# Kernel optimization log

Hardware: AMD Instinct MI355X
Metric: run time of the kernel (lower is better)

The kernel has to match this reference:

```python
import jax, jax.numpy as jnp
import numpy as np

N, E, D, K = 32768, 16384, 4, 8          # nodes, hyperedges, edges/node, nodes/edge
IN_DIM, OUT_DIM, EDGE_DIM, NUM_HEADS = 128, 128, 64, 8


def setup_inputs() -> dict:
    key = jax.random.key(0)
    ks = jax.random.split(key, 16)
    s_in = 1.0 / np.sqrt(IN_DIM)
    s_out = 1.0 / np.sqrt(OUT_DIM)
    s_edge = 1.0 / np.sqrt(EDGE_DIM)
    return {
        "x": jax.random.normal(ks[0], (N, IN_DIM), jnp.float32),
        "edge_attr": jax.random.normal(ks[1], (E, EDGE_DIM), jnp.float32),
        "node_edges": jax.random.randint(ks[2], (N, D), 0, E),   # hyperedges containing each node
        "edge_nodes": jax.random.randint(ks[3], (E, K), 0, N),   # nodes inside each hyperedge
        "W_lin": jax.random.normal(ks[4], (OUT_DIM, IN_DIM), jnp.float32) * s_in,
        "W_edge": jax.random.normal(ks[5], (OUT_DIM, EDGE_DIM), jnp.float32) * s_edge,
        "Wq": jax.random.normal(ks[6], (OUT_DIM, OUT_DIM), jnp.float32) * s_out,
        "Wk": jax.random.normal(ks[7], (OUT_DIM, OUT_DIM), jnp.float32) * s_out,
        "Wv": jax.random.normal(ks[8], (OUT_DIM, OUT_DIM), jnp.float32) * s_out,
        "bq": jnp.zeros((OUT_DIM,), jnp.float32),
        "bk": jnp.zeros((OUT_DIM,), jnp.float32),
        "bv": jnp.zeros((OUT_DIM,), jnp.float32),
        "Wo": jax.random.normal(ks[9], (OUT_DIM, OUT_DIM), jnp.float32) * s_out,
        "bo": jnp.zeros((OUT_DIM,), jnp.float32),
    }


def reference(x, edge_attr, node_edges, edge_nodes,
              W_lin, W_edge, Wq, Wk, Wv, bq, bk, bv, Wo, bo):
    n, out_dim = x.shape[0], W_lin.shape[0]
    hd = out_dim // NUM_HEADS
    L = node_edges.shape[1] * edge_nodes.shape[1]  # D*K keys per node

    Wh = x @ W_lin.T                               # [N, out]
    We = edge_attr @ W_edge.T                      # [E, out]

    u_idx = edge_nodes[node_edges]                 # [N, D, K] neighbor node ids
    vals = Wh[u_idx]                               # [N, D, K, out]
    keys = vals + We[node_edges][:, :, None, :]    # key = Wh[u] + We[e]
    keys = keys.reshape(n, L, out_dim)
    vals = vals.reshape(n, L, out_dim)

    # torch nn.MultiheadAttention: single query per node (query = Wh[v])
    q = (Wh @ Wq.T + bq).reshape(n, NUM_HEADS, hd)
    k = (keys @ Wk.T + bk).reshape(n, L, NUM_HEADS, hd)
    v = (vals @ Wv.T + bv).reshape(n, L, NUM_HEADS, hd)

    scores = jnp.einsum('nhd,nlhd->nhl', q, k) / jnp.sqrt(jnp.asarray(hd, q.dtype))
    attn = jax.nn.softmax(scores, axis=-1)         # [N, H, L]
    ctx = jnp.einsum('nhl,nlhd->nhd', attn, v).reshape(n, out_dim)
    out = ctx @ Wo.T + bo
    return jax.nn.relu(out)
```

## Files before the change

### kernel.cpp

```cpp
#include <hip/hip_runtime.h>

#define N_NODES 32768
#define N_EDGES 16384
#define DEG 4
#define KPE 8
#define DIM 128
#define EDIM 64
#define MAXC 64

typedef float f32x4 __attribute__((ext_vector_type(4)));
typedef __bf16 bf16x8 __attribute__((ext_vector_type(8)));
typedef __bf16 bf16x2 __attribute__((ext_vector_type(2)));
typedef unsigned short u16x8 __attribute__((ext_vector_type(8)));
typedef unsigned int u32;
typedef unsigned int u32x4 __attribute__((ext_vector_type(4)));
typedef int i32x4 __attribute__((ext_vector_type(4)));

static __device__ __forceinline__ unsigned short f2bf(float f) {
  union { float f; unsigned int u; } v; v.f = f;
  unsigned int r = (v.u + 0x7FFFu + ((v.u >> 16) & 1u)) >> 16;
  return (unsigned short)r;
}
static __device__ __forceinline__ float bflo(unsigned int v) {
  union { unsigned int u; float f; } x; x.u = v << 16; return x.f;
}
static __device__ __forceinline__ float bfhi(unsigned int v) {
  union { unsigned int u; float f; } x; x.u = v & 0xffff0000u; return x.f;
}
static __device__ __forceinline__ float f16tof(unsigned short h) {
  return (float)__builtin_bit_cast(_Float16, h);
}
static __device__ __forceinline__ unsigned short ftof16(float f) {
  return __builtin_bit_cast(unsigned short, (_Float16)f);
}

#if __has_builtin(__builtin_amdgcn_fdot2_f32_bf16)
static __device__ __forceinline__ float dot2bf(unsigned int a, unsigned int b, float c) {
  return __builtin_amdgcn_fdot2_f32_bf16(
      __builtin_bit_cast(bf16x2, a), __builtin_bit_cast(bf16x2, b), c, false);
}
#else
static __device__ __forceinline__ float dot2bf(unsigned int a, unsigned int b, float c) {
  c = fmaf(bflo(a), bflo(b), c);
  return fmaf(bfhi(a), bfhi(b), c);
}
#endif

__global__ __launch_bounds__(256) void zcnt_kernel(int* __restrict__ cnt)
{
  cnt[blockIdx.x * 256 + threadIdx.x] = 0;
}

__global__ __launch_bounds__(256) void wprep_kernel(
    const float* __restrict__ Wq, const float* __restrict__ Wk,
    const float* __restrict__ Wv, const float* __restrict__ Wlin,
    const float* __restrict__ Wedge, const float* __restrict__ Wo,
    const int* __restrict__ node_edges,
    unsigned short* __restrict__ CW, unsigned short* __restrict__ CWE,
    unsigned short* __restrict__ Wob, int* __restrict__ cnt, int* __restrict__ rev)
{
  int id = blockIdx.x * 256 + threadIdx.x;
  if (id < 384 * 128) {
    int j = id >> 7, i = id & 127;
    const float* wrow; float scale = 1.0f;
    if (j < 128)      { wrow = Wq + j * 128; scale = 0.25f; }
    else if (j < 256) { wrow = Wk + (j - 128) * 128; }
    else              { wrow = Wv + (j - 256) * 128; }
    float s = 0.f;
    #pragma unroll 8
    for (int m = 0; m < 128; ++m) s += wrow[m] * Wlin[m * 128 + i];
    CW[id] = f2bf(s * scale);
  } else if (id < 384 * 128 + 128 * 64) {
    int id2 = id - 384 * 128; int j = id2 >> 6, t = id2 & 63;
    float s = 0.f;
    #pragma unroll 8
    for (int m = 0; m < 128; ++m) s += Wk[j * 128 + m] * Wedge[m * 64 + t];
    CWE[id2] = f2bf(s);
  } else if (id < 384 * 128 + 128 * 64 + 128 * 128) {
    int id3 = id - (384 * 128 + 128 * 64);
    Wob[id3] = f2bf(Wo[id3]);
  } else {
    int t = id - (384 * 128 + 128 * 64 + 128 * 128);
    if (t < N_NODES * DEG) {
      int e = node_edges[t];
      int pos = atomicAdd(&cnt[e], 1);
      if (pos < MAXC) rev[(size_t)e * MAXC + pos] = t;
    }
  }
}

__global__ __launch_bounds__(256) void g12_kernel(
    const float* __restrict__ x, const unsigned short* __restrict__ CW,
    const float* __restrict__ bq, const float* __restrict__ bv,
    unsigned short* __restrict__ qb, unsigned short* __restrict__ Kb,
    unsigned short* __restrict__ Vb,
    const float* __restrict__ ea, const unsigned short* __restrict__ CWE,
    const float* __restrict__ bk, unsigned short* __restrict__ WeKb)
{
  const int wave = threadIdx.x >> 6, lane = threadIdx.x & 63;
  const int r16 = lane & 15, quad = lane >> 4;

  if (blockIdx.x < 512) {
    const int m0 = blockIdx.x * 64 + wave * 16;
    u16x8 av[4];
    const float* arow = x + (size_t)(m0 + r16) * DIM + quad * 8;
    #pragma unroll
    for (int kk = 0; kk < 4; ++kk) {
      float4 a0 = *(const float4*)(arow + kk * 32);
      float4 a1 = *(const float4*)(arow + kk * 32 + 4);
      u16x8 au;
      au[0] = f2bf(a0.x); au[1] = f2bf(a0.y); au[2] = f2bf(a0.z); au[3] = f2bf(a0.w);
      au[4] = f2bf(a1.x); au[5] = f2bf(a1.y); au[6] = f2bf(a1.z); au[7] = f2bf(a1.w);
      av[kk] = au;
    }
    #pragma unroll
    for (int g = 0; g < 6; ++g) {
      f32x4 acc[4];
      const f32x4 z = {0.f, 0.f, 0.f, 0.f};
      acc[0] = z; acc[1] = z; acc[2] = z; acc[3] = z;
      #pragma unroll
      for (int kk = 0; kk < 4; ++kk) {
        #pragma unroll
        for (int s = 0; s < 4; ++s) {
          u16x8 bu = *(const u16x8*)(CW + (size_t)(g * 64 + s * 16 + r16) * DIM + kk * 32 + quad * 8);
          acc[s] = __builtin_amdgcn_mfma_f32_16x16x32_bf16(
              __builtin_bit_cast(bf16x8, av[kk]), __builtin_bit_cast(bf16x8, bu), acc[s], 0, 0, 0);
        }
      }
      const int arr = g >> 1;
      const int colbase = (g & 1) * 64;
      unsigned short* dst = arr == 0 ? qb : (arr == 1 ? Kb : Vb);
      #pragma unroll
      for (int s = 0; s < 4; ++s) {
        int j = colbase + s * 16 + r16;
        float bias = arr == 0 ? 0.25f * bq[j] : (arr == 2 ? bv[j] : 0.f);
        #pragma unroll
        for (int r = 0; r < 4; ++r) {
          int m = m0 + quad * 4 + r;
          dst[(size_t)m * DIM + j] = f2bf(acc[s][r] + bias);
        }
      }
    }
  } else {
    const int idx = blockIdx.x - 512;
    const int m0 = (idx >> 1) * 64 + wave * 16;
    const int n0 = (idx & 1) * 64;
    f32x4 acc[4];
    const f32x4 z = {0.f, 0.f, 0.f, 0.f};
    acc[0] = z; acc[1] = z; acc[2] = z; acc[3] = z;
    const float* arow = ea + (size_t)(m0 + r16) * EDIM + quad * 8;
    #pragma unroll
    for (int kk = 0; kk < 2; ++kk) {
      float4 a0 = *(const float4*)(arow + kk * 32);
      float4 a1 = *(const float4*)(arow + kk * 32 + 4);
      u16x8 au;
      au[0] = f2bf(a0.x); au[1] = f2bf(a0.y); au[2] = f2bf(a0.z); au[3] = f2bf(a0.w);
      au[4] = f2bf(a1.x); au[5] = f2bf(a1.y); au[6] = f2bf(a1.z); au[7] = f2bf(a1.w);
      bf16x8 av = __builtin_bit_cast(bf16x8, au);
      #pragma unroll
      for (int s = 0; s < 4; ++s) {
        u16x8 bu = *(const u16x8*)(CWE + (size_t)(n0 + s * 16 + r16) * EDIM + kk * 32 + quad * 8);
        acc[s] = __builtin_amdgcn_mfma_f32_16x16x32_bf16(
            av, __builtin_bit_cast(bf16x8, bu), acc[s], 0, 0, 0);
      }
    }
    #pragma unroll
    for (int s = 0; s < 4; ++s) {
      int j = n0 + s * 16 + r16;
      float bias = bk[j];
      #pragma unroll
      for (int r = 0; r < 4; ++r) {
        int m = m0 + quad * 4 + r;
        WeKb[(size_t)m * DIM + j] = f2bf(acc[s][r] + bias);
      }
    }
  }
}

__global__ __launch_bounds__(256) void escore_kernel(
    const unsigned short* __restrict__ qb, const unsigned short* __restrict__ Kb,
    const unsigned short* __restrict__ WeKb, const int* __restrict__ enodes,
    const int* __restrict__ cnt, const int* __restrict__ rev,
    unsigned short* __restrict__ S)
{
  const int wave = threadIdx.x >> 6, lane = threadIdx.x & 63;
  const int e = blockIdx.x * 4 + wave;
  const int g = lane >> 3, j = lane & 7;

  int c_n = cnt[e]; if (c_n > MAXC) c_n = MAXC;
  if (c_n == 0) return;
  int rv = rev[(size_t)e * MAXC + lane];

  int mid = enodes[(size_t)e * KPE + g];
  u32x4 k0 = *(const u32x4*)(Kb + (size_t)mid * DIM + j * 16);
  u32x4 k1 = *(const u32x4*)(Kb + (size_t)mid * DIM + j * 16 + 8);
  u32x4 w0 = *(const u32x4*)(WeKb + (size_t)e * DIM + j * 16);
  u32x4 w1 = *(const u32x4*)(WeKb + (size_t)e * DIM + j * 16 + 8);

  int pk = __shfl(rv, 0);
  u32x4 qa0 = *(const u32x4*)(qb + (size_t)(pk >> 2) * DIM + j * 16);
  u32x4 qa1 = *(const u32x4*)(qb + (size_t)(pk >> 2) * DIM + j * 16 + 8);

  for (int c = 0; c < c_n; ++c) {
    const int n = pk >> 2, d = pk & 3;
    u32x4 q0 = qa0, q1 = qa1;
    if (c + 1 < c_n) {
      pk = __shfl(rv, c + 1);
      qa0 = *(const u32x4*)(qb + (size_t)(pk >> 2) * DIM + j * 16);
      qa1 = *(const u32x4*)(qb + (size_t)(pk >> 2) * DIM + j * 16 + 8);
    }
    float s = 0.f;
    s = dot2bf(q0.x, k0.x, s); s = dot2bf(q0.y, k0.y, s);
    s = dot2bf(q0.z, k0.z, s); s = dot2bf(q0.w, k0.w, s);
    s = dot2bf(q1.x, k1.x, s); s = dot2bf(q1.y, k1.y, s);
    s = dot2bf(q1.z, k1.z, s); s = dot2bf(q1.w, k1.w, s);
    s = dot2bf(q0.x, w0.x, s); s = dot2bf(q0.y, w0.y, s);
    s = dot2bf(q0.z, w0.z, s); s = dot2bf(q0.w, w0.w, s);
    s = dot2bf(q1.x, w1.x, s); s = dot2bf(q1.y, w1.y, s);
    s = dot2bf(q1.z, w1.z, s); s = dot2bf(q1.w, w1.w, s);
    S[(size_t)n * 256 + d * 64 + g * 8 + j] = ftof16(s);
  }
}

__global__ __launch_bounds__(256) void nsm_kernel(unsigned short* __restrict__ SP)
{
  const int wave = threadIdx.x >> 6, lane = threadIdx.x & 63;
  const int n = blockIdx.x * 4 + wave;
  const int l = lane & 31, hp = lane >> 5;
  unsigned short* row = SP + (size_t)n * 256;

  uint2 sv = *(const uint2*)(row + l * 8 + hp * 4);
  float s4[4] = { f16tof(sv.x & 0xffff), f16tof(sv.x >> 16),
                  f16tof(sv.y & 0xffff), f16tof(sv.y >> 16) };
  unsigned short pr[4];
  #pragma unroll
  for (int hi = 0; hi < 4; ++hi) {
    float vmax = s4[hi];
    #pragma unroll
    for (int off = 16; off >= 1; off >>= 1)
      vmax = fmaxf(vmax, __shfl_xor(vmax, off, 32));
    float ex = __expf(s4[hi] - vmax);
    float sum = ex;
    #pragma unroll
    for (int off = 16; off >= 1; off >>= 1)
      sum += __shfl_xor(sum, off, 32);
    pr[hi] = ftof16(ex / sum);
  }
  #pragma unroll
  for (int hi = 0; hi < 4; ++hi)
    row[(hp * 4 + hi) * 32 + l] = pr[hi];
}

__global__ __launch_bounds__(256) void ectx_kernel(
    const unsigned short* __restrict__ Vb, const unsigned short* __restrict__ P,
    const int* __restrict__ enodes, const int* __restrict__ cnt,
    const int* __restrict__ rev, unsigned short* __restrict__ ctxp)
{
  const int wave = threadIdx.x >> 6, lane = threadIdx.x & 63;
  const int e = blockIdx.x * 4 + wave;
  const int c0 = lane * 2, h = lane >> 3;

  int c_n = cnt[e]; if (c_n > MAXC) c_n = MAXC;
  if (c_n == 0) return;
  int rv = rev[(size_t)e * MAXC + lane];

  const int* ep = enodes + (size_t)e * KPE;
  i32x4 a4 = *(const i32x4*)ep;
  i32x4 b4 = *(const i32x4*)(ep + 4);
  int id[8] = {a4.x, a4.y, a4.z, a4.w, b4.x, b4.y, b4.z, b4.w};
  u32 vv[8];
  #pragma unroll
  for (int k = 0; k < 8; ++k) vv[k] = *(const u32*)(Vb + (size_t)id[k] * DIM + c0);

  int pk = __shfl(rv, 0);
  uint4 pva = *(const uint4*)(P + (size_t)(pk >> 2) * 256 + h * 32 + (pk & 3) * 8);

  for (int c = 0; c < c_n; ++c) {
    const int n = pk >> 2, d = pk & 3;
    uint4 pv = pva;
    if (c + 1 < c_n) {
      pk = __shfl(rv, c + 1);
      pva = *(const uint4*)(P + (size_t)(pk >> 2) * 256 + h * 32 + (pk & 3) * 8);
    }
    float p0 = f16tof(pv.x & 0xffff), p1 = f16tof(pv.x >> 16);
    float p2 = f16tof(pv.y & 0xffff), p3 = f16tof(pv.y >> 16);
    float p4 = f16tof(pv.z & 0xffff), p5 = f16tof(pv.z >> 16);
    float p6 = f16tof(pv.w & 0xffff), p7 = f16tof(pv.w >> 16);
    float a0 = 0.f, a1 = 0.f;
    a0 = fmaf(p0, bflo(vv[0]), a0); a1 = fmaf(p0, bfhi(vv[0]), a1);
    a0 = fmaf(p1, bflo(vv[1]), a0); a1 = fmaf(p1, bfhi(vv[1]), a1);
    a0 = fmaf(p2, bflo(vv[2]), a0); a1 = fmaf(p2, bfhi(vv[2]), a1);
    a0 = fmaf(p3, bflo(vv[3]), a0); a1 = fmaf(p3, bfhi(vv[3]), a1);
    a0 = fmaf(p4, bflo(vv[4]), a0); a1 = fmaf(p4, bfhi(vv[4]), a1);
    a0 = fmaf(p5, bflo(vv[5]), a0); a1 = fmaf(p5, bfhi(vv[5]), a1);
    a0 = fmaf(p6, bflo(vv[6]), a0); a1 = fmaf(p6, bfhi(vv[6]), a1);
    a0 = fmaf(p7, bflo(vv[7]), a0); a1 = fmaf(p7, bfhi(vv[7]), a1);
    u32 pk2 = (u32)ftof16(a0) | ((u32)ftof16(a1) << 16);
    *(u32*)(ctxp + ((size_t)n * 4 + d) * DIM + c0) = pk2;
  }
}

__global__ __launch_bounds__(256) void g4_kernel(
    const unsigned short* __restrict__ ctxp, const unsigned short* __restrict__ Wob,
    const float* __restrict__ bo, float* __restrict__ out)
{
  const int wave = threadIdx.x >> 6, lane = threadIdx.x & 63;
  const int r16 = lane & 15, quad = lane >> 4;
  const int m0 = blockIdx.x * 64 + wave * 16;

  f32x4 acc[2][4];
  const f32x4 z = {0.f, 0.f, 0.f, 0.f};
  #pragma unroll
  for (int hf = 0; hf < 2; ++hf) { acc[hf][0] = z; acc[hf][1] = z; acc[hf][2] = z; acc[hf][3] = z; }

  #pragma unroll
  for (int kk = 0; kk < 4; ++kk) {
    float fa[8] = {0.f, 0.f, 0.f, 0.f, 0.f, 0.f, 0.f, 0.f};
    #pragma unroll
    for (int d = 0; d < 4; ++d) {
      u16x8 t = *(const u16x8*)(ctxp + ((size_t)(m0 + r16) * 4 + d) * DIM + kk * 32 + quad * 8);
      #pragma unroll
      for (int i = 0; i < 8; ++i) fa[i] += f16tof(t[i]);
    }
    u16x8 au;
    #pragma unroll
    for (int i = 0; i < 8; ++i) au[i] = f2bf(fa[i]);
    bf16x8 av = __builtin_bit_cast(bf16x8, au);
    #pragma unroll
    for (int hf = 0; hf < 2; ++hf) {
      #pragma unroll
      for (int s = 0; s < 4; ++s) {
        u16x8 bu = *(const u16x8*)(Wob + (size_t)(hf * 64 + s * 16 + r16) * DIM + kk * 32 + quad * 8);
        acc[hf][s] = __builtin_amdgcn_mfma_f32_16x16x32_bf16(
            av, __builtin_bit_cast(bf16x8, bu), acc[hf][s], 0, 0, 0);
      }
    }
  }

  #pragma unroll
  for (int hf = 0; hf < 2; ++hf) {
    #pragma unroll
    for (int s = 0; s < 4; ++s) {
      int jj = hf * 64 + s * 16 + r16;
      float bias = bo[jj];
      #pragma unroll
      for (int r = 0; r < 4; ++r) {
        int m = m0 + quad * 4 + r;
        float v = acc[hf][s][r] + bias;
        out[(size_t)m * DIM + jj] = v > 0.f ? v : 0.f;
      }
    }
  }
}

extern "C" void kernel_launch(void* const* d_in, const int* in_sizes, int n_in,
                              void* d_out, int out_size, void* d_ws, size_t ws_size,
                              hipStream_t stream)
{
  const float* x     = (const float*)d_in[0];
  const float* ea    = (const float*)d_in[1];
  const int* nedges  = (const int*)d_in[2];
  const int* enodes  = (const int*)d_in[3];
  const float* Wlin  = (const float*)d_in[4];
  const float* Wedge = (const float*)d_in[5];
  const float* Wq    = (const float*)d_in[6];
  const float* Wk    = (const float*)d_in[7];
  const float* Wv    = (const float*)d_in[8];
  const float* bq    = (const float*)d_in[9];
  const float* bk    = (const float*)d_in[10];
  const float* bv    = (const float*)d_in[11];
  const float* Wo    = (const float*)d_in[12];
  const float* bo    = (const float*)d_in[13];
  float* out = (float*)d_out;

  unsigned short* wsp = (unsigned short*)d_ws;
  unsigned short* CW   = wsp;  wsp += 384 * 128;
  unsigned short* CWE  = wsp;  wsp += 128 * 64;
  unsigned short* Wob  = wsp;  wsp += 128 * 128;
  unsigned short* qb   = wsp;  wsp += (size_t)N_NODES * DIM;
  unsigned short* Kb   = wsp;  wsp += (size_t)N_NODES * DIM;
  unsigned short* Vb   = wsp;  wsp += (size_t)N_NODES * DIM;
  unsigned short* WeKb = wsp;  wsp += (size_t)N_EDGES * DIM;
  unsigned short* SP   = wsp;  wsp += (size_t)N_NODES * 256;
  unsigned short* ctxp = wsp;  wsp += (size_t)N_NODES * 4 * DIM;
  int* cnt = (int*)wsp;        wsp += N_EDGES * 2;
  int* rev = (int*)wsp;        wsp += (size_t)N_EDGES * MAXC * 2;

  zcnt_kernel<<<dim3(64), dim3(256), 0, stream>>>(cnt);
  wprep_kernel<<<dim3(800), dim3(256), 0, stream>>>(
      Wq, Wk, Wv, Wlin, Wedge, Wo, nedges, CW, CWE, Wob, cnt, rev);
  g12_kernel<<<dim3(1024), dim3(256), 0, stream>>>(x, CW, bq, bv, qb, Kb, Vb, ea, CWE, bk, WeKb);
  escore_kernel<<<dim3(N_EDGES / 4), dim3(256), 0, stream>>>(qb, Kb, WeKb, enodes, cnt, rev, SP);
  nsm_kernel<<<dim3(N_NODES / 4), dim3(256), 0, stream>>>(SP);
  ectx_kernel<<<dim3(N_EDGES / 4), dim3(256), 0, stream>>>(Vb, SP, enodes, cnt, rev, ctxp);
  g4_kernel<<<dim3(512), dim3(256), 0, stream>>>(ctxp, Wob, bo, out);
}
```

Measured before the change: 207.5 us.

## Swap MFMA operands for vectorized epilogue stores and batch gather loads

The MFMA A/B operands are swapped in the projection, edge and output GEMMs, so each lane's accumulator holds four consecutive output columns of one row. Each lane can then write a packed 8-byte bf16 or 16-byte float4 store with a vector bias load, replacing scattered 2-byte and 4-byte writes. The escore and context gather loops now issue eight independent q/P row loads per batch before computing, instead of prefetching only one row ahead, to expose more memory-level parallelism. This raises register pressure and does some wasted loads on padded tail iterations.

```diff
diff --git a/kernel.cpp b/kernel.cpp
--- a/kernel.cpp
+++ b/kernel.cpp
@@ -124,21 +124,27 @@
         for (int s = 0; s < 4; ++s) {
           u16x8 bu = *(const u16x8*)(CW + (size_t)(g * 64 + s * 16 + r16) * DIM + kk * 32 + quad * 8);
           acc[s] = __builtin_amdgcn_mfma_f32_16x16x32_bf16(
-              __builtin_bit_cast(bf16x8, av[kk]), __builtin_bit_cast(bf16x8, bu), acc[s], 0, 0, 0);
+              __builtin_bit_cast(bf16x8, bu), __builtin_bit_cast(bf16x8, av[kk]), acc[s], 0, 0, 0);
         }
       }
       const int arr = g >> 1;
       const int colbase = (g & 1) * 64;
       unsigned short* dst = arr == 0 ? qb : (arr == 1 ? Kb : Vb);
+      const int m = m0 + r16;
       #pragma unroll
       for (int s = 0; s < 4; ++s) {
-        int j = colbase + s * 16 + r16;
-        float bias = arr == 0 ? 0.25f * bq[j] : (arr == 2 ? bv[j] : 0.f);
-        #pragma unroll
-        for (int r = 0; r < 4; ++r) {
-          int m = m0 + quad * 4 + r;
-          dst[(size_t)m * DIM + j] = f2bf(acc[s][r] + bias);
+        const int j0 = colbase + s * 16 + quad * 4;
+        float4 b4 = {0.f, 0.f, 0.f, 0.f};
+        if (arr == 0) {
+          float4 t = *(const float4*)(bq + j0);
+          b4.x = 0.25f * t.x; b4.y = 0.25f * t.y; b4.z = 0.25f * t.z; b4.w = 0.25f * t.w;
+        } else if (arr == 2) {
+          b4 = *(const float4*)(bv + j0);
         }
+        u32 lo = (u32)f2bf(acc[s][0] + b4.x) | ((u32)f2bf(acc[s][1] + b4.y) << 16);
+        u32 hi = (u32)f2bf(acc[s][2] + b4.z) | ((u32)f2bf(acc[s][3] + b4.w) << 16);
+        uint2 st = {lo, hi};
+        *(uint2*)(dst + (size_t)m * DIM + j0) = st;
       }
     }
   } else {
@@ -161,18 +167,18 @@
       for (int s = 0; s < 4; ++s) {
         u16x8 bu = *(const u16x8*)(CWE + (size_t)(n0 + s * 16 + r16) * EDIM + kk * 32 + quad * 8);
         acc[s] = __builtin_amdgcn_mfma_f32_16x16x32_bf16(
-            av, __builtin_bit_cast(bf16x8, bu), acc[s], 0, 0, 0);
-      }
-    }
+            __builtin_bit_cast(bf16x8, bu), av, acc[s], 0, 0, 0);
+      }
+    }
+    const int m = m0 + r16;
     #pragma unroll
     for (int s = 0; s < 4; ++s) {
-      int j = n0 + s * 16 + r16;
-      float bias = bk[j];
-      #pragma unroll
-      for (int r = 0; r < 4; ++r) {
-        int m = m0 + quad * 4 + r;
-        WeKb[(size_t)m * DIM + j] = f2bf(acc[s][r] + bias);
-      }
+      const int j0 = n0 + s * 16 + quad * 4;
+      float4 b4 = *(const float4*)(bk + j0);
+      u32 lo = (u32)f2bf(acc[s][0] + b4.x) | ((u32)f2bf(acc[s][1] + b4.y) << 16);
+      u32 hi = (u32)f2bf(acc[s][2] + b4.z) | ((u32)f2bf(acc[s][3] + b4.w) << 16);
+      uint2 st = {lo, hi};
+      *(uint2*)(WeKb + (size_t)m * DIM + j0) = st;
     }
   }
 }
@@ -197,28 +203,32 @@
   u32x4 w0 = *(const u32x4*)(WeKb + (size_t)e * DIM + j * 16);
   u32x4 w1 = *(const u32x4*)(WeKb + (size_t)e * DIM + j * 16 + 8);
 
-  int pk = __shfl(rv, 0);
-  u32x4 qa0 = *(const u32x4*)(qb + (size_t)(pk >> 2) * DIM + j * 16);
-  u32x4 qa1 = *(const u32x4*)(qb + (size_t)(pk >> 2) * DIM + j * 16 + 8);
-
-  for (int c = 0; c < c_n; ++c) {
-    const int n = pk >> 2, d = pk & 3;
-    u32x4 q0 = qa0, q1 = qa1;
-    if (c + 1 < c_n) {
-      pk = __shfl(rv, c + 1);
-      qa0 = *(const u32x4*)(qb + (size_t)(pk >> 2) * DIM + j * 16);
-      qa1 = *(const u32x4*)(qb + (size_t)(pk >> 2) * DIM + j * 16 + 8);
-    }
-    float s = 0.f;
-    s = dot2bf(q0.x, k0.x, s); s = dot2bf(q0.y, k0.y, s);
-    s = dot2bf(q0.z, k0.z, s); s = dot2bf(q0.w, k0.w, s);
-    s = dot2bf(q1.x, k1.x, s); s = dot2bf(q1.y, k1.y, s);
-    s = dot2bf(q1.z, k1.z, s); s = dot2bf(q1.w, k1.w, s);
-    s = dot2bf(q0.x, w0.x, s); s = dot2bf(q0.y, w0.y, s);
-    s = dot2bf(q0.z, w0.z, s); s = dot2bf(q0.w, w0.w, s);
-    s = dot2bf(q1.x, w1.x, s); s = dot2bf(q1.y, w1.y, s);
-    s = dot2bf(q1.z, w1.z, s); s = dot2bf(q1.w, w1.w, s);
-    S[(size_t)n * 256 + d * 64 + g * 8 + j] = ftof16(s);
+  for (int base = 0; base < c_n; base += 8) {
+    int pks[8];
+    u32x4 q0[8], q1[8];
+    #pragma unroll
+    for (int i = 0; i < 8; ++i) {
+      int pk = __shfl(rv, base + i);
+      pks[i] = (base + i < c_n) ? pk : 0;
+      const unsigned short* qr = qb + (size_t)(pks[i] >> 2) * DIM + j * 16;
+      q0[i] = *(const u32x4*)qr;
+      q1[i] = *(const u32x4*)(qr + 8);
+    }
+    #pragma unroll
+    for (int i = 0; i < 8; ++i) {
+      if (base + i < c_n) {
+        float s = 0.f;
+        s = dot2bf(q0[i].x, k0.x, s); s = dot2bf(q0[i].y, k0.y, s);
+        s = dot2bf(q0[i].z, k0.z, s); s = dot2bf(q0[i].w, k0.w, s);
+        s = dot2bf(q1[i].x, k1.x, s); s = dot2bf(q1[i].y, k1.y, s);
+        s = dot2bf(q1[i].z, k1.z, s); s = dot2bf(q1[i].w, k1.w, s);
+        s = dot2bf(q0[i].x, w0.x, s); s = dot2bf(q0[i].y, w0.y, s);
+        s = dot2bf(q0[i].z, w0.z, s); s = dot2bf(q0[i].w, w0.w, s);
+        s = dot2bf(q1[i].x, w1.x, s); s = dot2bf(q1[i].y, w1.y, s);
+        s = dot2bf(q1[i].z, w1.z, s); s = dot2bf(q1[i].w, w1.w, s);
+        S[(size_t)(pks[i] >> 2) * 256 + (pks[i] & 3) * 64 + g * 8 + j] = ftof16(s);
+      }
+    }
   }
 }
 
@@ -272,31 +282,35 @@
   #pragma unroll
   for (int k = 0; k < 8; ++k) vv[k] = *(const u32*)(Vb + (size_t)id[k] * DIM + c0);
 
-  int pk = __shfl(rv, 0);
-  uint4 pva = *(const uint4*)(P + (size_t)(pk >> 2) * 256 + h * 32 + (pk & 3) * 8);
-
-  for (int c = 0; c < c_n; ++c) {
-    const int n = pk >> 2, d = pk & 3;
-    uint4 pv = pva;
-    if (c + 1 < c_n) {
-      pk = __shfl(rv, c + 1);
-      pva = *(const uint4*)(P + (size_t)(pk >> 2) * 256 + h * 32 + (pk & 3) * 8);
-    }
-    float p0 = f16tof(pv.x & 0xffff), p1 = f16tof(pv.x >> 16);
-    float p2 = f16tof(pv.y & 0xffff), p3 = f16tof(pv.y >> 16);
-    float p4 = f16tof(pv.z & 0xffff), p5 = f16tof(pv.z >> 16);
-    float p6 = f16tof(pv.w & 0xffff), p7 = f16tof(pv.w >> 16);
-    float a0 = 0.f, a1 = 0.f;
-    a0 = fmaf(p0, bflo(vv[0]), a0); a1 = fmaf(p0, bfhi(vv[0]), a1);
-    a0 = fmaf(p1, bflo(vv[1]), a0); a1 = fmaf(p1, bfhi(vv[1]), a1);
-    a0 = fmaf(p2, bflo(vv[2]), a0); a1 = fmaf(p2, bfhi(vv[2]), a1);
-    a0 = fmaf(p3, bflo(vv[3]), a0); a1 = fmaf(p3, bfhi(vv[3]), a1);
-    a0 = fmaf(p4, bflo(vv[4]), a0); a1 = fmaf(p4, bfhi(vv[4]), a1);
-    a0 = fmaf(p5, bflo(vv[5]), a0); a1 = fmaf(p5, bfhi(vv[5]), a1);
-    a0 = fmaf(p6, bflo(vv[6]), a0); a1 = fmaf(p6, bfhi(vv[6]), a1);
-    a0 = fmaf(p7, bflo(vv[7]), a0); a1 = fmaf(p7, bfhi(vv[7]), a1);
-    u32 pk2 = (u32)ftof16(a0) | ((u32)ftof16(a1) << 16);
-    *(u32*)(ctxp + ((size_t)n * 4 + d) * DIM + c0) = pk2;
+  for (int base = 0; base < c_n; base += 8) {
+    int pks[8];
+    uint4 pv[8];
+    #pragma unroll
+    for (int i = 0; i < 8; ++i) {
+      int pk = __shfl(rv, base + i);
+      pks[i] = (base + i < c_n) ? pk : 0;
+      pv[i] = *(const uint4*)(P + (size_t)(pks[i] >> 2) * 256 + h * 32 + (pks[i] & 3) * 8);
+    }
+    #pragma unroll
+    for (int i = 0; i < 8; ++i) {
+      if (base + i < c_n) {
+        float p0 = f16tof(pv[i].x & 0xffff), p1 = f16tof(pv[i].x >> 16);
+        float p2 = f16tof(pv[i].y & 0xffff), p3 = f16tof(pv[i].y >> 16);
+        float p4 = f16tof(pv[i].z & 0xffff), p5 = f16tof(pv[i].z >> 16);
+        float p6 = f16tof(pv[i].w & 0xffff), p7 = f16tof(pv[i].w >> 16);
+        float a0 = 0.f, a1 = 0.f;
+        a0 = fmaf(p0, bflo(vv[0]), a0); a1 = fmaf(p0, bfhi(vv[0]), a1);
+        a0 = fmaf(p1, bflo(vv[1]), a0); a1 = fmaf(p1, bfhi(vv[1]), a1);
+        a0 = fmaf(p2, bflo(vv[2]), a0); a1 = fmaf(p2, bfhi(vv[2]), a1);
+        a0 = fmaf(p3, bflo(vv[3]), a0); a1 = fmaf(p3, bfhi(vv[3]), a1);
+        a0 = fmaf(p4, bflo(vv[4]), a0); a1 = fmaf(p4, bfhi(vv[4]), a1);
+        a0 = fmaf(p5, bflo(vv[5]), a0); a1 = fmaf(p5, bfhi(vv[5]), a1);
+        a0 = fmaf(p6, bflo(vv[6]), a0); a1 = fmaf(p6, bfhi(vv[6]), a1);
+        a0 = fmaf(p7, bflo(vv[7]), a0); a1 = fmaf(p7, bfhi(vv[7]), a1);
+        u32 pk2 = (u32)ftof16(a0) | ((u32)ftof16(a1) << 16);
+        *(u32*)(ctxp + ((size_t)(pks[i] >> 2) * 4 + (pks[i] & 3)) * DIM + c0) = pk2;
+      }
+    }
   }
 }
 
@@ -332,23 +346,24 @@
       for (int s = 0; s < 4; ++s) {
         u16x8 bu = *(const u16x8*)(Wob + (size_t)(hf * 64 + s * 16 + r16) * DIM + kk * 32 + quad * 8);
         acc[hf][s] = __builtin_amdgcn_mfma_f32_16x16x32_bf16(
-            av, __builtin_bit_cast(bf16x8, bu), acc[hf][s], 0, 0, 0);
-      }
-    }
-  }
-
+            __builtin_bit_cast(bf16x8, bu), av, acc[hf][s], 0, 0, 0);
+      }
+    }
+  }
+
+  const int m = m0 + r16;
   #pragma unroll
   for (int hf = 0; hf < 2; ++hf) {
     #pragma unroll
     for (int s = 0; s < 4; ++s) {
-      int jj = hf * 64 + s * 16 + r16;
-      float bias = bo[jj];
-      #pragma unroll
-      for (int r = 0; r < 4; ++r) {
-        int m = m0 + quad * 4 + r;
-        float v = acc[hf][s][r] + bias;
-        out[(size_t)m * DIM + jj] = v > 0.f ? v : 0.f;
-      }
+      const int j0 = hf * 64 + s * 16 + quad * 4;
+      float4 b4 = *(const float4*)(bo + j0);
+      float4 v;
+      v.x = acc[hf][s][0] + b4.x; v.x = v.x > 0.f ? v.x : 0.f;
+      v.y = acc[hf][s][1] + b4.y; v.y = v.y > 0.f ? v.y : 0.f;
+      v.z = acc[hf][s][2] + b4.z; v.z = v.z > 0.f ? v.z : 0.f;
+      v.w = acc[hf][s][3] + b4.w; v.w = v.w > 0.f ? v.w : 0.f;
+      *(float4*)(out + (size_t)m * DIM + j0) = v;
     }
   }
 }
```

After: 217.6 us. +4.8%, slower.

## Accumulate per-node context with fp16 atomics and vectorize GEMM epilogue stores

Applied to the files above, without the earlier changes.

The per-(node, edge-slot) context partials are replaced by direct packed fp16x2 atomic adds into a single per-node context buffer, which is zeroed in the init kernel. The output GEMM no longer has to read and sum four partials, which cuts context buffer traffic by a factor of four. The MFMA operands are also swapped so each lane holds four consecutive columns, letting the epilogues write packed uint2/float4 stores instead of scattered scalar stores. The cost is atomic contention, nondeterministic fp16 summation order, and a larger zeroing kernel.

```diff
diff --git a/kernel.cpp b/kernel.cpp
--- a/kernel.cpp
+++ b/kernel.cpp
@@ -46,9 +46,39 @@
 }
 #endif
 
-__global__ __launch_bounds__(256) void zcnt_kernel(int* __restrict__ cnt)
-{
-  cnt[blockIdx.x * 256 + threadIdx.x] = 0;
+static __device__ __forceinline__ void atomAddF16x2(unsigned short* p, u32 val) {
+#if __has_builtin(__builtin_amdgcn_global_atomic_fadd_v2f16)
+  typedef _Float16 hf2 __attribute__((ext_vector_type(2)));
+  __builtin_amdgcn_global_atomic_fadd_v2f16(
+      (__attribute__((address_space(1))) hf2*)p, __builtin_bit_cast(hf2, val));
+#else
+  u32* q = (u32*)p;
+  u32 old = *q, assumed;
+  do {
+    assumed = old;
+    _Float16 lo = __builtin_bit_cast(_Float16, (unsigned short)(assumed & 0xffff)) +
+                  __builtin_bit_cast(_Float16, (unsigned short)(val & 0xffff));
+    _Float16 hi = __builtin_bit_cast(_Float16, (unsigned short)(assumed >> 16)) +
+                  __builtin_bit_cast(_Float16, (unsigned short)(val >> 16));
+    u32 nv = (u32)__builtin_bit_cast(unsigned short, lo) |
+             ((u32)__builtin_bit_cast(unsigned short, hi) << 16);
+    old = atomicCAS(q, assumed, nv);
+  } while (old != assumed);
+#endif
+}
+
+__global__ __launch_bounds__(256) void zcnt_kernel(int* __restrict__ cnt,
+                                                   unsigned short* __restrict__ ctx)
+{
+  int id = blockIdx.x * 256 + threadIdx.x;
+  if (id < N_EDGES / 4) {
+    i32x4 z = {0, 0, 0, 0};
+    ((i32x4*)cnt)[id] = z;
+  }
+  if (id < (N_NODES * DIM) / 8) {
+    u32x4 z = {0, 0, 0, 0};
+    ((u32x4*)ctx)[id] = z;
+  }
 }
 
 __global__ __launch_bounds__(256) void wprep_kernel(
@@ -124,21 +154,27 @@
         for (int s = 0; s < 4; ++s) {
           u16x8 bu = *(const u16x8*)(CW + (size_t)(g * 64 + s * 16 + r16) * DIM + kk * 32 + quad * 8);
           acc[s] = __builtin_amdgcn_mfma_f32_16x16x32_bf16(
-              __builtin_bit_cast(bf16x8, av[kk]), __builtin_bit_cast(bf16x8, bu), acc[s], 0, 0, 0);
+              __builtin_bit_cast(bf16x8, bu), __builtin_bit_cast(bf16x8, av[kk]), acc[s], 0, 0, 0);
         }
       }
       const int arr = g >> 1;
       const int colbase = (g & 1) * 64;
       unsigned short* dst = arr == 0 ? qb : (arr == 1 ? Kb : Vb);
+      const int m = m0 + r16;
       #pragma unroll
       for (int s = 0; s < 4; ++s) {
-        int j = colbase + s * 16 + r16;
-        float bias = arr == 0 ? 0.25f * bq[j] : (arr == 2 ? bv[j] : 0.f);
-        #pragma unroll
-        for (int r = 0; r < 4; ++r) {
-          int m = m0 + quad * 4 + r;
-          dst[(size_t)m * DIM + j] = f2bf(acc[s][r] + bias);
+        const int j0 = colbase + s * 16 + quad * 4;
+        float4 b4 = {0.f, 0.f, 0.f, 0.f};
+        if (arr == 0) {
+          float4 t = *(const float4*)(bq + j0);
+          b4.x = 0.25f * t.x; b4.y = 0.25f * t.y; b4.z = 0.25f * t.z; b4.w = 0.25f * t.w;
+        } else if (arr == 2) {
+          b4 = *(const float4*)(bv + j0);
         }
+        u32 lo = (u32)f2bf(acc[s][0] + b4.x) | ((u32)f2bf(acc[s][1] + b4.y) << 16);
+        u32 hi = (u32)f2bf(acc[s][2] + b4.z) | ((u32)f2bf(acc[s][3] + b4.w) << 16);
+        uint2 st = {lo, hi};
+        *(uint2*)(dst + (size_t)m * DIM + j0) = st;
       }
     }
   } else {
@@ -161,18 +197,18 @@
       for (int s = 0; s < 4; ++s) {
         u16x8 bu = *(const u16x8*)(CWE + (size_t)(n0 + s * 16 + r16) * EDIM + kk * 32 + quad * 8);
         acc[s] = __builtin_amdgcn_mfma_f32_16x16x32_bf16(
-            av, __builtin_bit_cast(bf16x8, bu), acc[s], 0, 0, 0);
+            __builtin_bit_cast(bf16x8, bu), av, acc[s], 0, 0, 0);
       }
     }
+    const int m = m0 + r16;
     #pragma unroll
     for (int s = 0; s < 4; ++s) {
-      int j = n0 + s * 16 + r16;
-      float bias = bk[j];
-      #pragma unroll
-      for (int r = 0; r < 4; ++r) {
-        int m = m0 + quad * 4 + r;
-        WeKb[(size_t)m * DIM + j] = f2bf(acc[s][r] + bias);
-      }
+      const int j0 = n0 + s * 16 + quad * 4;
+      float4 b4 = *(const float4*)(bk + j0);
+      u32 lo = (u32)f2bf(acc[s][0] + b4.x) | ((u32)f2bf(acc[s][1] + b4.y) << 16);
+      u32 hi = (u32)f2bf(acc[s][2] + b4.z) | ((u32)f2bf(acc[s][3] + b4.w) << 16);
+      uint2 st = {lo, hi};
+      *(uint2*)(WeKb + (size_t)m * DIM + j0) = st;
     }
   }
 }
@@ -254,7 +290,7 @@
 __global__ __launch_bounds__(256) void ectx_kernel(
     const unsigned short* __restrict__ Vb, const unsigned short* __restrict__ P,
     const int* __restrict__ enodes, const int* __restrict__ cnt,
-    const int* __restrict__ rev, unsigned short* __restrict__ ctxp)
+    const int* __restrict__ rev, unsigned short* __restrict__ ctx)
 {
   const int wave = threadIdx.x >> 6, lane = threadIdx.x & 63;
   const int e = blockIdx.x * 4 + wave;
@@ -276,7 +312,7 @@
   uint4 pva = *(const uint4*)(P + (size_t)(pk >> 2) * 256 + h * 32 + (pk & 3) * 8);
 
   for (int c = 0; c < c_n; ++c) {
-    const int n = pk >> 2, d = pk & 3;
+    const int n = pk >> 2;
     uint4 pv = pva;
     if (c + 1 < c_n) {
       pk = __shfl(rv, c + 1);
@@ -296,12 +332,12 @@
     a0 = fmaf(p6, bflo(vv[6]), a0); a1 = fmaf(p6, bfhi(vv[6]), a1);
     a0 = fmaf(p7, bflo(vv[7]), a0); a1 = fmaf(p7, bfhi(vv[7]), a1);
     u32 pk2 = (u32)ftof16(a0) | ((u32)ftof16(a1) << 16);
-    *(u32*)(ctxp + ((size_t)n * 4 + d) * DIM + c0) = pk2;
+    atomAddF16x2(ctx + (size_t)n * DIM + c0, pk2);
   }
 }
 
 __global__ __launch_bounds__(256) void g4_kernel(
-    const unsigned short* __restrict__ ctxp, const unsigned short* __restrict__ Wob,
+    const unsigned short* __restrict__ ctx, const unsigned short* __restrict__ Wob,
     const float* __restrict__ bo, float* __restrict__ out)
 {
   const int wave = threadIdx.x >> 6, lane = threadIdx.x & 63;
@@ -315,16 +351,10 @@
 
   #pragma unroll
   for (int kk = 0; kk < 4; ++kk) {
-    float fa[8] = {0.f, 0.f, 0.f, 0.f, 0.f, 0.f, 0.f, 0.f};
-    #pragma unroll
-    for (int d = 0; d < 4; ++d) {
-      u16x8 t = *(const u16x8*)(ctxp + ((size_t)(m0 + r16) * 4 + d) * DIM + kk * 32 + quad * 8);
-      #pragma unroll
-      for (int i = 0; i < 8; ++i) fa[i] += f16tof(t[i]);
-    }
+    u16x8 t = *(const u16x8*)(ctx + (size_t)(m0 + r16) * DIM + kk * 32 + quad * 8);
     u16x8 au;
     #pragma unroll
-    for (int i = 0; i < 8; ++i) au[i] = f2bf(fa[i]);
+    for (int i = 0; i < 8; ++i) au[i] = f2bf(f16tof(t[i]));
     bf16x8 av = __builtin_bit_cast(bf16x8, au);
     #pragma unroll
     for (int hf = 0; hf < 2; ++hf) {
@@ -332,23 +362,24 @@
       for (int s = 0; s < 4; ++s) {
         u16x8 bu = *(const u16x8*)(Wob + (size_t)(hf * 64 + s * 16 + r16) * DIM + kk * 32 + quad * 8);
         acc[hf][s] = __builtin_amdgcn_mfma_f32_16x16x32_bf16(
-            av, __builtin_bit_cast(bf16x8, bu), acc[hf][s], 0, 0, 0);
+            __builtin_bit_cast(bf16x8, bu), av, acc[hf][s], 0, 0, 0);
       }
     }
   }
 
+  const int m = m0 + r16;
   #pragma unroll
   for (int hf = 0; hf < 2; ++hf) {
     #pragma unroll
     for (int s = 0; s < 4; ++s) {
-      int jj = hf * 64 + s * 16 + r16;
-      float bias = bo[jj];
-      #pragma unroll
-      for (int r = 0; r < 4; ++r) {
-        int m = m0 + quad * 4 + r;
-        float v = acc[hf][s][r] + bias;
-        out[(size_t)m * DIM + jj] = v > 0.f ? v : 0.f;
-      }
+      const int j0 = hf * 64 + s * 16 + quad * 4;
+      float4 b4 = *(const float4*)(bo + j0);
+      float4 v;
+      v.x = acc[hf][s][0] + b4.x; v.x = v.x > 0.f ? v.x : 0.f;
+      v.y = acc[hf][s][1] + b4.y; v.y = v.y > 0.f ? v.y : 0.f;
+      v.z = acc[hf][s][2] + b4.z; v.z = v.z > 0.f ? v.z : 0.f;
+      v.w = acc[hf][s][3] + b4.w; v.w = v.w > 0.f ? v.w : 0.f;
+      *(float4*)(out + (size_t)m * DIM + j0) = v;
     }
   }
 }
@@ -382,16 +413,16 @@
   unsigned short* Vb   = wsp;  wsp += (size_t)N_NODES * DIM;
   unsigned short* WeKb = wsp;  wsp += (size_t)N_EDGES * DIM;
   unsigned short* SP   = wsp;  wsp += (size_t)N_NODES * 256;
-  unsigned short* ctxp = wsp;  wsp += (size_t)N_NODES * 4 * DIM;
+  unsigned short* ctx  = wsp;  wsp += (size_t)N_NODES * DIM;
   int* cnt = (int*)wsp;        wsp += N_EDGES * 2;
   int* rev = (int*)wsp;        wsp += (size_t)N_EDGES * MAXC * 2;
 
-  zcnt_kernel<<<dim3(64), dim3(256), 0, stream>>>(cnt);
+  zcnt_kernel<<<dim3(2048), dim3(256), 0, stream>>>(cnt, ctx);
   wprep_kernel<<<dim3(800), dim3(256), 0, stream>>>(
       Wq, Wk, Wv, Wlin, Wedge, Wo, nedges, CW, CWE, Wob, cnt, rev);
   g12_kernel<<<dim3(1024), dim3(256), 0, stream>>>(x, CW, bq, bv, qb, Kb, Vb, ea, CWE, bk, WeKb);
   escore_kernel<<<dim3(N_EDGES / 4), dim3(256), 0, stream>>>(qb, Kb, WeKb, enodes, cnt, rev, SP);
   nsm_kernel<<<dim3(N_NODES / 4), dim3(256), 0, stream>>>(SP);
-  ectx_kernel<<<dim3(N_EDGES / 4), dim3(256), 0, stream>>>(Vb, SP, enodes, cnt, rev, ctxp);
-  g4_kernel<<<dim3(512), dim3(256), 0, stream>>>(ctxp, Wob, bo, out);
-}
+  ectx_kernel<<<dim3(N_EDGES / 4), dim3(256), 0, stream>>>(Vb, SP, enodes, cnt, rev, ctx);
+  g4_kernel<<<dim3(512), dim3(256), 0, stream>>>(ctx, Wob, bo, out);
+}
```

Measured after the change: 225.4 us. 1.09x slower.
